# Kernel tuning notes

Measured on AMD Instinct MI355X. Metric: run time of the kernel, lower is better.

The kernel has to match this reference:

```python
import jax, jax.numpy as jnp
import numpy as np

NA, NPAPER, IN, HID, H, D, OUT, E = 16384, 16384, 128, 64, 4, 16, 349, 262144
NEG_SLOPE = 0.2  # DGL GATConv default leaky_relu slope


def _gat(hs, hd, src, dst, W, al, ar, b, n_dst):
    # DGL GATConv: shared fc, additive attention, edge softmax per dst, weighted sum.
    fs = (hs @ W).reshape(-1, H, D)            # [Ns,H,D]
    fd = (hd @ W).reshape(-1, H, D)            # [Nd,H,D]
    el = jnp.sum(fs * al, axis=-1)             # [Ns,H]
    er = jnp.sum(fd * ar, axis=-1)             # [Nd,H]
    e = jax.nn.leaky_relu(el[src] + er[dst], NEG_SLOPE)  # [E,H]
    m = jax.ops.segment_max(e, dst, num_segments=n_dst)
    m = jnp.where(jnp.isfinite(m), m, 0.0)
    ex = jnp.exp(e - m[dst])
    den = jax.ops.segment_sum(ex, dst, num_segments=n_dst)
    alpha = ex / jnp.maximum(den[dst], 1e-9)   # [E,H]
    out = jax.ops.segment_sum(fs[src] * alpha[..., None], dst, num_segments=n_dst)
    return out + b.reshape(1, H, D)


def _ln(x, g, b):
    m = jnp.mean(x, -1, keepdims=True)
    v = jnp.mean((x - m) ** 2, -1, keepdims=True)
    return (x - m) / jnp.sqrt(v + 1e-5) * g + b


def setup_inputs() -> dict:
    key = jax.random.key(0)
    ks = jax.random.split(key, 30)
    def n(k, shp, s=1.0):
        return jax.random.normal(ks[k], shp, jnp.float32) * s
    def ridx(k, hi):
        return jax.random.randint(ks[k], (E,), 0, hi)
    return dict(
        x_author=n(0, (NA, IN)), x_paper=n(1, (NPAPER, IN)),
        ntype_emb=n(2, (2, IN), 0.5),
        W0=n(3, (3, IN, HID), 0.1), al0=n(4, (3, H, D), 0.1), ar0=n(5, (3, H, D), 0.1), b0=jnp.zeros((3, HID), jnp.float32),
        W1=n(6, (3, HID, HID), 0.1), al1=n(7, (3, H, D), 0.1), ar1=n(8, (3, H, D), 0.1), b1=jnp.zeros((3, HID), jnp.float32),
        ln1_gb=jnp.array([1.0, 0.0], jnp.float32),
        attn_w=n(9, (4,), 0.5), attn_b=n(10, (4,), 0.1),
        ln2_gb=jnp.array([1.0, 0.0], jnp.float32),
        ffn_w1=n(11, (1, 16), 0.5), ffn_b1=jnp.zeros((16,), jnp.float32),
        ffn_w2=n(12, (16, 1), 0.5), ffn_b2=jnp.zeros((1,), jnp.float32),
        lin_W=n(13, (2 * HID, OUT), 0.1), lin_b=jnp.zeros((OUT,), jnp.float32),
        src_writes=ridx(14, NA), dst_writes=ridx(15, NPAPER),
        src_cites=ridx(16, NPAPER), dst_cites=ridx(17, NPAPER),
        src_revw=ridx(18, NPAPER), dst_revw=ridx(19, NA),
    )


def reference(x_author, x_paper, ntype_emb, W0, al0, ar0, b0, W1, al1, ar1, b1,
              ln1_gb, attn_w, attn_b, ln2_gb, ffn_w1, ffn_b1, ffn_w2, ffn_b2,
              lin_W, lin_b,
              src_writes, dst_writes, src_cites, dst_cites, src_revw, dst_revw):
    # node-type embedding scaling (x[nty] * ntype_emb[i])
    ha = x_author * ntype_emb[0]
    hp = x_paper * ntype_emb[1]

    def hetero(ha, hp, W, al, ar, b):
        # HeteroGraphConv with sum aggregation over etypes per dst ntype
        op = _gat(ha, hp, src_writes, dst_writes, W[0], al[0], ar[0], b[0], NPAPER) \
           + _gat(hp, hp, src_cites, dst_cites, W[1], al[1], ar[1], b[1], NPAPER)
        oa = _gat(hp, ha, src_revw, dst_revw, W[2], al[2], ar[2], b[2], NA)
        return oa.reshape(NA, HID), op.reshape(NPAPER, HID)

    ha, hp = hetero(ha, hp, W0, al0, ar0, b0)
    ha, hp = jax.nn.relu(ha), jax.nn.relu(hp)  # dropout = identity at eval
    ha, hp = hetero(ha, hp, W1, al1, ar1, b1)

    h1 = hp                                   # [NP, HID]
    x = h1[:, :, None]                        # [NP, HID, 1]: feature dims as tokens, d=1
    # DALayer (pre-LN transformer encoder layer, 1 head, d=1, scale=1)
    y = _ln(x, ln1_gb[0], ln1_gb[1])
    q = y * attn_w[0] + attn_b[0]
    k = y * attn_w[1] + attn_b[1]
    v = y * attn_w[2] + attn_b[2]
    att = jax.nn.softmax(jnp.einsum('nsd,ntd->nst', q, k), axis=-1)  # [NP,HID,HID]
    o = jnp.einsum('nst,ntd->nsd', att, v) * attn_w[3] + attn_b[3]
    x = x + o
    y = _ln(x, ln2_gb[0], ln2_gb[1])
    f = jax.nn.gelu(y @ ffn_w1 + ffn_b1, approximate=False) @ ffn_w2 + ffn_b2
    x = x + f
    h2 = x[:, :, 0]                           # squeeze

    def l2n(z):
        return z / jnp.maximum(jnp.linalg.norm(z, axis=1, keepdims=True), 1e-12)

    hf = jnp.concatenate([l2n(h1), l2n(h2)], axis=1)  # [NP, 2*HID]
    return hf @ lin_W + lin_b
```

## Files before the change

kernel.cpp:

```cpp
#include <hip/hip_runtime.h>
#include <math.h>

constexpr int N_A   = 16384;
constexpr int N_P   = 16384;
constexpr int IN_D  = 128;
constexpr int HID   = 64;
constexpr int NH    = 4;
constexpr int OUTD  = 349;
constexpr int NE    = 262144;
constexpr int NB    = 64;
constexpr float NEG = 0.2f;

__device__ __forceinline__ float lrelu(float x) { return x > 0.f ? x : NEG * x; }

__global__ __launch_bounds__(256) void k_chist(const int* __restrict__ dW, const int* __restrict__ dC,
                                               const int* __restrict__ dR, int* __restrict__ ccnt) {
    __shared__ int h[256];
    const int t = blockIdx.y;
    const int* __restrict__ d = t == 0 ? dW : t == 1 ? dC : dR;
    const int tid = threadIdx.x;
    h[tid] = 0;
    __syncthreads();
    const int base = blockIdx.x * 4096;
#pragma unroll
    for (int i = 0; i < 16; ++i) {
        int dst = d[base + i * 256 + tid];
        atomicAdd(&h[dst >> 6], 1);
    }
    __syncthreads();
    ccnt[(t * NB + blockIdx.x) * 256 + tid] = h[tid];
}

__global__ __launch_bounds__(768) void k_coffs(const int* __restrict__ ccnt, int* __restrict__ coffs,
                                               int* __restrict__ crow) {
    const int tid = threadIdx.x;
    const int t = tid >> 8, bin = tid & 255;
    int total = 0;
    for (int b = 0; b < NB; ++b) total += ccnt[(t * NB + b) * 256 + bin];
    __shared__ int sc[768];
    sc[tid] = total;
    __syncthreads();
    for (int w = 1; w < 256; w <<= 1) {
        int v = (bin >= w) ? sc[tid - w] : 0;
        __syncthreads();
        sc[tid] += v;
        __syncthreads();
    }
    const int incl = sc[tid];
    const int base = incl - total;
    crow[t * 257 + bin] = base;
    if (bin == 255) crow[t * 257 + 256] = incl;
    int run = base;
    for (int b = 0; b < NB; ++b) {
        int c = ccnt[(t * NB + b) * 256 + bin];
        coffs[(t * NB + b) * 256 + bin] = run;
        run += c;
    }
}

__global__ __launch_bounds__(256) void k_cscatter(const int* __restrict__ sW, const int* __restrict__ dW,
                                                  const int* __restrict__ sC, const int* __restrict__ dC,
                                                  const int* __restrict__ sR, const int* __restrict__ dR,
                                                  const int* __restrict__ coffs,
                                                  int* __restrict__ ebW, int* __restrict__ ebC,
                                                  int* __restrict__ ebR) {
    __shared__ int cur[256];
    const int t = blockIdx.y;
    const int* __restrict__ sp = t == 0 ? sW : t == 1 ? sC : sR;
    const int* __restrict__ dp = t == 0 ? dW : t == 1 ? dC : dR;
    int* __restrict__ eb = t == 0 ? ebW : t == 1 ? ebC : ebR;
    const int tid = threadIdx.x;
    cur[tid] = coffs[(t * NB + blockIdx.x) * 256 + tid];
    __syncthreads();
    const int base = blockIdx.x * 4096;
#pragma unroll
    for (int i = 0; i < 16; ++i) {
        int e = base + i * 256 + tid;
        int dst = dp[e], src = sp[e];
        int pos = atomicAdd(&cur[dst >> 6], 1);
        eb[pos] = src | ((dst & 63) << 14);
    }
}

__global__ __launch_bounds__(256) void k_fine(const int* __restrict__ crow,
                                              const int* __restrict__ ebW, const int* __restrict__ ebC,
                                              const int* __restrict__ ebR,
                                              int* __restrict__ row,
                                              int* __restrict__ esW, int* __restrict__ esC,
                                              int* __restrict__ esR) {
    __shared__ int bins[64], exc[64], cur[64];
    const int t = blockIdx.y, cb = blockIdx.x, tid = threadIdx.x;
    const int* __restrict__ eb = t == 0 ? ebW : t == 1 ? ebC : ebR;
    int* __restrict__ es = t == 0 ? esW : t == 1 ? esC : esR;
    const int lo = crow[t * 257 + cb], hi = crow[t * 257 + cb + 1];
    if (tid < 64) bins[tid] = 0;
    __syncthreads();
    for (int e = lo + tid; e < hi; e += 256) atomicAdd(&bins[eb[e] >> 14], 1);
    __syncthreads();
    if (tid == 0) {
        int r = 0;
#pragma unroll
        for (int j = 0; j < 64; ++j) { exc[j] = r; cur[j] = r; r += bins[j]; }
    }
    __syncthreads();
    if (tid < 64) row[t * 16385 + cb * 64 + tid] = lo + exc[tid];
    if (tid == 0 && cb == 255) row[t * 16385 + 16384] = crow[t * 257 + 256];
    for (int e = lo + tid; e < hi; e += 256) {
        int v = eb[e];
        int pos = atomicAdd(&cur[v >> 14], 1);
        es[lo + pos] = v & 16383;
    }
}

struct GemmJobs {
    const float* X[5];  const float* W[5];  const float* NT[5];
    float* F[5];        float* EL[5];       float* ER[5];
    const float* AL[5]; const float* AR[5];
};

template <int K, int RELU>
__global__ __launch_bounds__(256) void k_gemm(GemmJobs j) {
    __shared__ float Wc[32 * 64];
    __shared__ float XT[32][68];

    const float* __restrict__ X;  const float* __restrict__ Wp;  const float* __restrict__ NTp;
    float* __restrict__ F;  float* __restrict__ EL;  float* __restrict__ ER;
    const float* __restrict__ AL; const float* __restrict__ AR;
    switch (blockIdx.z) {
      case 0: X=j.X[0]; Wp=j.W[0]; NTp=j.NT[0]; F=j.F[0]; EL=j.EL[0]; ER=j.ER[0]; AL=j.AL[0]; AR=j.AR[0]; break;
      case 1: X=j.X[1]; Wp=j.W[1]; NTp=j.NT[1]; F=j.F[1]; EL=j.EL[1]; ER=j.ER[1]; AL=j.AL[1]; AR=j.AR[1]; break;
      case 2: X=j.X[2]; Wp=j.W[2]; NTp=j.NT[2]; F=j.F[2]; EL=j.EL[2]; ER=j.ER[2]; AL=j.AL[2]; AR=j.AR[2]; break;
      case 3: X=j.X[3]; Wp=j.W[3]; NTp=j.NT[3]; F=j.F[3]; EL=j.EL[3]; ER=j.ER[3]; AL=j.AL[3]; AR=j.AR[3]; break;
      default: X=j.X[4]; Wp=j.W[4]; NTp=j.NT[4]; F=j.F[4]; EL=j.EL[4]; ER=j.ER[4]; AL=j.AL[4]; AR=j.AR[4]; break;
    }

    const int tid = threadIdx.x;
    const int tx  = tid & 15;
    const int rg  = tid >> 4;
    const int r0  = blockIdx.x * 64;

    float acc[4][4] = {};

    for (int kc = 0; kc < K; kc += 32) {
        __syncthreads();
#pragma unroll
        for (int it = 0; it < 2; ++it) {
            int idx = tid * 4 + it * 1024;
            int k = idx >> 6, c = idx & 63;
            *(float4*)(Wc + idx) = *(const float4*)(Wp + (size_t)(kc + k) * 64 + c);
        }
#pragma unroll
        for (int it = 0; it < 2; ++it) {
            int idx = tid * 4 + it * 1024;
            int row = idx >> 5, col = idx & 31;
            float4 v = *(const float4*)(X + (size_t)(r0 + row) * K + kc + col);
            if (RELU) {
                v.x = fmaxf(v.x, 0.f); v.y = fmaxf(v.y, 0.f);
                v.z = fmaxf(v.z, 0.f); v.w = fmaxf(v.w, 0.f);
            }
            if (NTp) {
                float4 s = *(const float4*)(NTp + kc + col);
                v.x *= s.x; v.y *= s.y; v.z *= s.z; v.w *= s.w;
            }
            XT[col + 0][row] = v.x;
            XT[col + 1][row] = v.y;
            XT[col + 2][row] = v.z;
            XT[col + 3][row] = v.w;
        }
        __syncthreads();
#pragma unroll
        for (int kk = 0; kk < 32; ++kk) {
            float4 a4 = *(const float4*)(&XT[kk][rg * 4]);
            float4 w4 = *(const float4*)(Wc + kk * 64 + tx * 4);
            acc[0][0] = fmaf(a4.x, w4.x, acc[0][0]); acc[0][1] = fmaf(a4.x, w4.y, acc[0][1]);
            acc[0][2] = fmaf(a4.x, w4.z, acc[0][2]); acc[0][3] = fmaf(a4.x, w4.w, acc[0][3]);
            acc[1][0] = fmaf(a4.y, w4.x, acc[1][0]); acc[1][1] = fmaf(a4.y, w4.y, acc[1][1]);
            acc[1][2] = fmaf(a4.y, w4.z, acc[1][2]); acc[1][3] = fmaf(a4.y, w4.w, acc[1][3]);
            acc[2][0] = fmaf(a4.z, w4.x, acc[2][0]); acc[2][1] = fmaf(a4.z, w4.y, acc[2][1]);
            acc[2][2] = fmaf(a4.z, w4.z, acc[2][2]); acc[2][3] = fmaf(a4.z, w4.w, acc[2][3]);
            acc[3][0] = fmaf(a4.w, w4.x, acc[3][0]); acc[3][1] = fmaf(a4.w, w4.y, acc[3][1]);
            acc[3][2] = fmaf(a4.w, w4.z, acc[3][2]); acc[3][3] = fmaf(a4.w, w4.w, acc[3][3]);
        }
    }

    if (F) {
#pragma unroll
        for (int i = 0; i < 4; ++i) {
            size_t n = (size_t)r0 + rg * 4 + i;
            *(float4*)(F + n * 64 + tx * 4) =
                make_float4(acc[i][0], acc[i][1], acc[i][2], acc[i][3]);
        }
    }
    if (EL) {
        float4 alv = ((const float4*)AL)[tx];
#pragma unroll
        for (int i = 0; i < 4; ++i) {
            float p = acc[i][0] * alv.x + acc[i][1] * alv.y +
                      acc[i][2] * alv.z + acc[i][3] * alv.w;
            p += __shfl_xor(p, 1, 64);
            p += __shfl_xor(p, 2, 64);
            if ((tx & 3) == 0) EL[((size_t)r0 + rg * 4 + i) * 4 + (tx >> 2)] = p;
        }
    }
    if (ER) {
        float4 arv = ((const float4*)AR)[tx];
#pragma unroll
        for (int i = 0; i < 4; ++i) {
            float p = acc[i][0] * arv.x + acc[i][1] * arv.y +
                      acc[i][2] * arv.z + acc[i][3] * arv.w;
            p += __shfl_xor(p, 1, 64);
            p += __shfl_xor(p, 2, 64);
            if ((tx & 3) == 0) ER[((size_t)r0 + rg * 4 + i) * 4 + (tx >> 2)] = p;
        }
    }
}

struct AggType { const int* row; const int* es; const float* el; const float* er; const float* fs; };
struct AggArgs {
    AggType t[3]; const float* b; float* op; float* oa;
    float* hf;
    const float* ln1gb; const float* aw; const float* ab; const float* ln2gb;
    const float* fw1; const float* fb1; const float* fw2; const float* fb2;
};

__device__ __forceinline__ float4 agg16v(const int* __restrict__ rowv, const int* __restrict__ es,
                                         const float* __restrict__ el, const float* __restrict__ er,
                                         const float* __restrict__ fs, int d, int lane,
                                         float* denOut) {
    float4 acc = make_float4(0.f, 0.f, 0.f, 0.f);
    float den = 0.f;
    int start = rowv[d], deg = rowv[d + 1] - start;
    if (deg > 0) {
        const int j16 = lane & 15;
        const int g   = lane >> 4;
        const int h   = j16 >> 2;
        const float rh = er[(size_t)d * 4 + g];
        for (int e0 = 0; e0 < deg; e0 += 16) {
            int o = e0 + j16;
            int sn = es[start + (o < deg ? o : 0)];
            float wv = 0.f;
            if (o < deg) wv = __expf(lrelu(el[(size_t)sn * 4 + g] + rh));
            den += wv;
#pragma unroll
            for (int sub = 0; sub < 4; ++sub) {
                int eidx = sub * 4 + g;
                int snj  = __shfl(sn, eidx, 64);
                float wj = __shfl(wv, (h << 4) + eidx, 64);
                float4 f4 = *(const float4*)(fs + (size_t)snj * 64 + j16 * 4);
                acc.x = fmaf(wj, f4.x, acc.x);
                acc.y = fmaf(wj, f4.y, acc.y);
                acc.z = fmaf(wj, f4.z, acc.z);
                acc.w = fmaf(wj, f4.w, acc.w);
            }
        }
    }
    *denOut = den;
    return acc;
}

__device__ __forceinline__ float4 agg_finish(float4 acc, float den, int lane) {
#pragma unroll
    for (int w = 1; w < 16; w <<= 1) den += __shfl_xor(den, w, 64);
#pragma unroll
    for (int w = 16; w < 64; w <<= 1) {
        acc.x += __shfl_xor(acc.x, w, 64);
        acc.y += __shfl_xor(acc.y, w, 64);
        acc.z += __shfl_xor(acc.z, w, 64);
        acc.w += __shfl_xor(acc.w, w, 64);
    }
    float denh = __shfl(den, (((lane & 15) >> 2) << 4), 64);
    float inv = 1.f / fmaxf(denh, 1e-9f);
    acc.x *= inv; acc.y *= inv; acc.z *= inv; acc.w *= inv;
    return acc;
}

template <int L1>
__global__ __launch_bounds__(256) void k_agg(AggArgs A) {
    int wid = (blockIdx.x * 256 + threadIdx.x) >> 6;
    int lane = threadIdx.x & 63;
    int c16 = lane & 15;
    if (L1 == 0) {
        if (wid < N_P) {
            float d0, d1;
            float4 a0 = agg16v(A.t[0].row, A.t[0].es, A.t[0].el, A.t[0].er, A.t[0].fs, wid, lane, &d0);
            float4 a1 = agg16v(A.t[1].row, A.t[1].es, A.t[1].el, A.t[1].er, A.t[1].fs, wid, lane, &d1);
            a0 = agg_finish(a0, d0, lane);
            a1 = agg_finish(a1, d1, lane);
            if (lane < 16) {
                float4 b0 = *(const float4*)(A.b + c16 * 4);
                float4 b1 = *(const float4*)(A.b + 64 + c16 * 4);
                float4 o = make_float4(a0.x + a1.x + b0.x + b1.x,
                                       a0.y + a1.y + b0.y + b1.y,
                                       a0.z + a1.z + b0.z + b1.z,
                                       a0.w + a1.w + b0.w + b1.w);
                *(float4*)(A.op + (size_t)wid * 64 + c16 * 4) = o;
            }
        } else {
            int d = wid - N_P;
            float d2;
            float4 a2 = agg16v(A.t[2].row, A.t[2].es, A.t[2].el, A.t[2].er, A.t[2].fs, d, lane, &d2);
            a2 = agg_finish(a2, d2, lane);
            if (lane < 16) {
                float4 b2 = *(const float4*)(A.b + 128 + c16 * 4);
                float4 o = make_float4(a2.x + b2.x, a2.y + b2.y, a2.z + b2.z, a2.w + b2.w);
                *(float4*)(A.oa + (size_t)d * 64 + c16 * 4) = o;
            }
        }
    } else {
        float d0, d1;
        float4 a0 = agg16v(A.t[0].row, A.t[0].es, A.t[0].el, A.t[0].er, A.t[0].fs, wid, lane, &d0);
        float4 a1 = agg16v(A.t[1].row, A.t[1].es, A.t[1].el, A.t[1].er, A.t[1].fs, wid, lane, &d1);
        a0 = agg_finish(a0, d0, lane);
        a1 = agg_finish(a1, d1, lane);
        float4 b0 = *(const float4*)(A.b + c16 * 4);
        float4 b1 = *(const float4*)(A.b + 64 + c16 * 4);
        float4 o = make_float4(a0.x + a1.x + b0.x + b1.x,
                               a0.y + a1.y + b0.y + b1.y,
                               a0.z + a1.z + b0.z + b1.z,
                               a0.w + a1.w + b0.w + b1.w);
        float y1 = A.ln1gb[1];
        float vv = y1 * A.aw[2] + A.ab[2];
        float oo = vv * A.aw[3] + A.ab[3];
        float y2 = A.ln2gb[1];
        float f  = A.fb2[0];
#pragma unroll
        for (int q = 0; q < 16; ++q) {
            float zz = y2 * A.fw1[q] + A.fb1[q];
            f += 0.5f * zz * (1.f + erff(zz * 0.70710678118654752f)) * A.fw2[q];
        }
        float C = oo + f;
        float4 oc = make_float4(o.x + C, o.y + C, o.z + C, o.w + C);
        float s1 = o.x * o.x + o.y * o.y + o.z * o.z + o.w * o.w;
        float s2 = oc.x * oc.x + oc.y * oc.y + oc.z * oc.z + oc.w * oc.w;
#pragma unroll
        for (int w = 1; w < 16; w <<= 1) {
            s1 += __shfl_xor(s1, w, 64);
            s2 += __shfl_xor(s2, w, 64);
        }
        float i1 = 1.f / fmaxf(sqrtf(s1), 1e-12f);
        float i2 = 1.f / fmaxf(sqrtf(s2), 1e-12f);
        if (lane < 16) {
            *(float4*)(A.hf + (size_t)wid * 128 + c16 * 4) =
                make_float4(o.x * i1, o.y * i1, o.z * i1, o.w * i1);
            *(float4*)(A.hf + (size_t)wid * 128 + 64 + c16 * 4) =
                make_float4(oc.x * i2, oc.y * i2, oc.z * i2, oc.w * i2);
        }
    }
}

__global__ __launch_bounds__(256) void k_gemm_out(const float* __restrict__ X,
                                                  const float* __restrict__ W,
                                                  const float* __restrict__ bias,
                                                  float* __restrict__ out) {
    __shared__ float Wc[32 * 64];
    __shared__ float XT[32][68];
    const int tid = threadIdx.x;
    const int tx  = tid & 15;
    const int rg  = tid >> 4;
    const int r0  = blockIdx.x * 64;
    const int c0  = blockIdx.y * 64;

    float acc[4][4] = {};

    for (int kc = 0; kc < 128; kc += 32) {
        __syncthreads();
#pragma unroll
        for (int it = 0; it < 2; ++it) {
            int idx = tid * 4 + it * 1024;
            int k = idx >> 6, c = idx & 63;
            int gk = kc + k;
            float4 v;
            int gc = c0 + c;
            v.x = (gc + 0 < OUTD) ? W[(size_t)gk * OUTD + gc + 0] : 0.f;
            v.y = (gc + 1 < OUTD) ? W[(size_t)gk * OUTD + gc + 1] : 0.f;
            v.z = (gc + 2 < OUTD) ? W[(size_t)gk * OUTD + gc + 2] : 0.f;
            v.w = (gc + 3 < OUTD) ? W[(size_t)gk * OUTD + gc + 3] : 0.f;
            *(float4*)(Wc + idx) = v;
        }
#pragma unroll
        for (int it = 0; it < 2; ++it) {
            int idx = tid * 4 + it * 1024;
            int row = idx >> 5, col = idx & 31;
            float4 v = *(const float4*)(X + (size_t)(r0 + row) * 128 + kc + col);
            XT[col + 0][row] = v.x;
            XT[col + 1][row] = v.y;
            XT[col + 2][row] = v.z;
            XT[col + 3][row] = v.w;
        }
        __syncthreads();
#pragma unroll
        for (int kk = 0; kk < 32; ++kk) {
            float4 a4 = *(const float4*)(&XT[kk][rg * 4]);
            float4 w4 = *(const float4*)(Wc + kk * 64 + tx * 4);
            acc[0][0] = fmaf(a4.x, w4.x, acc[0][0]); acc[0][1] = fmaf(a4.x, w4.y, acc[0][1]);
            acc[0][2] = fmaf(a4.x, w4.z, acc[0][2]); acc[0][3] = fmaf(a4.x, w4.w, acc[0][3]);
            acc[1][0] = fmaf(a4.y, w4.x, acc[1][0]); acc[1][1] = fmaf(a4.y, w4.y, acc[1][1]);
            acc[1][2] = fmaf(a4.y, w4.z, acc[1][2]); acc[1][3] = fmaf(a4.y, w4.w, acc[1][3]);
            acc[2][0] = fmaf(a4.z, w4.x, acc[2][0]); acc[2][1] = fmaf(a4.z, w4.y, acc[2][1]);
            acc[2][2] = fmaf(a4.z, w4.z, acc[2][2]); acc[2][3] = fmaf(a4.z, w4.w, acc[2][3]);
            acc[3][0] = fmaf(a4.w, w4.x, acc[3][0]); acc[3][1] = fmaf(a4.w, w4.y, acc[3][1]);
            acc[3][2] = fmaf(a4.w, w4.z, acc[3][2]); acc[3][3] = fmaf(a4.w, w4.w, acc[3][3]);
        }
    }

    float b4[4];
#pragma unroll
    for (int q = 0; q < 4; ++q) {
        int c = c0 + tx * 4 + q;
        b4[q] = (c < OUTD) ? bias[c] : 0.f;
    }
#pragma unroll
    for (int i = 0; i < 4; ++i) {
        size_t n = (size_t)r0 + rg * 4 + i;
#pragma unroll
        for (int q = 0; q < 4; ++q) {
            int c = c0 + tx * 4 + q;
            if (c < OUTD) out[n * OUTD + c] = acc[i][q] + b4[q];
        }
    }
}

extern "C" void kernel_launch(void* const* d_in, const int* in_sizes, int n_in,
                              void* d_out, int out_size, void* d_ws, size_t ws_size,
                              hipStream_t stream) {
    const float* x_author = (const float*)d_in[0];
    const float* x_paper  = (const float*)d_in[1];
    const float* ntype    = (const float*)d_in[2];
    const float* W0  = (const float*)d_in[3];
    const float* al0 = (const float*)d_in[4];
    const float* ar0 = (const float*)d_in[5];
    const float* b0  = (const float*)d_in[6];
    const float* W1  = (const float*)d_in[7];
    const float* al1 = (const float*)d_in[8];
    const float* ar1 = (const float*)d_in[9];
    const float* b1  = (const float*)d_in[10];
    const float* ln1gb = (const float*)d_in[11];
    const float* attw  = (const float*)d_in[12];
    const float* attb  = (const float*)d_in[13];
    const float* ln2gb = (const float*)d_in[14];
    const float* fw1 = (const float*)d_in[15];
    const float* fb1 = (const float*)d_in[16];
    const float* fw2 = (const float*)d_in[17];
    const float* fb2 = (const float*)d_in[18];
    const float* linW = (const float*)d_in[19];
    const float* linb = (const float*)d_in[20];
    const int* srcW = (const int*)d_in[21];
    const int* dstW = (const int*)d_in[22];
    const int* srcC = (const int*)d_in[23];
    const int* dstC = (const int*)d_in[24];
    const int* srcR = (const int*)d_in[25];
    const int* dstR = (const int*)d_in[26];
    float* out = (float*)d_out;

    float* ws = (float*)d_ws;
    size_t off = 0;
    float* fsW = ws + off; off += (size_t)N_A * HID;
    float* fsC = ws + off; off += (size_t)N_P * HID;
    float* fsR = ws + off; off += (size_t)N_P * HID;
    float* elw = ws + off; off += (size_t)N_A * NH;
    float* erw = ws + off; off += (size_t)N_P * NH;
    float* elc = ws + off; off += (size_t)N_P * NH;
    float* erc = ws + off; off += (size_t)N_P * NH;
    float* elr = ws + off; off += (size_t)N_P * NH;
    float* err = ws + off; off += (size_t)N_A * NH;
    float* oa0 = ws + off; off += (size_t)N_A * HID;
    float* op0 = ws + off; off += (size_t)N_P * HID;
    float* hf  = ws + off; off += (size_t)N_P * 2 * HID;
    int* ccnt  = (int*)(ws + off); off += 3 * NB * 256;
    int* coffs = (int*)(ws + off); off += 3 * NB * 256;
    int* crow  = (int*)(ws + off); off += 3 * 257 + 1;
    int* row   = (int*)(ws + off); off += 3 * 16385 + 1;
    int* ebW  = (int*)(ws + off); off += NE;
    int* ebC  = (int*)(ws + off); off += NE;
    int* ebR  = (int*)(ws + off); off += NE;
    int* esW  = (int*)(ws + off); off += NE;
    int* esC  = (int*)(ws + off); off += NE;
    int* esR  = (int*)(ws + off); off += NE;

    const int* rowW = row;
    const int* rowC = row + 16385;
    const int* rowR = row + 2 * 16385;

    const float* ntA = ntype;
    const float* ntP = ntype + IN_D;

    GemmJobs j0{};
    j0.X[0] = x_author; j0.W[0] = W0;                  j0.NT[0] = ntA;
    j0.F[0] = fsW; j0.EL[0] = elw; j0.ER[0] = nullptr; j0.AL[0] = al0;       j0.AR[0] = nullptr;
    j0.X[1] = x_paper;  j0.W[1] = W0;                  j0.NT[1] = ntP;
    j0.F[1] = nullptr; j0.EL[1] = nullptr; j0.ER[1] = erw; j0.AL[1] = nullptr; j0.AR[1] = ar0;
    j0.X[2] = x_paper;  j0.W[2] = W0 + IN_D * HID;     j0.NT[2] = ntP;
    j0.F[2] = fsC; j0.EL[2] = elc; j0.ER[2] = erc;     j0.AL[2] = al0 + 64;  j0.AR[2] = ar0 + 64;
    j0.X[3] = x_paper;  j0.W[3] = W0 + 2 * IN_D * HID; j0.NT[3] = ntP;
    j0.F[3] = fsR; j0.EL[3] = elr; j0.ER[3] = nullptr; j0.AL[3] = al0 + 128; j0.AR[3] = nullptr;
    j0.X[4] = x_author; j0.W[4] = W0 + 2 * IN_D * HID; j0.NT[4] = ntA;
    j0.F[4] = nullptr; j0.EL[4] = nullptr; j0.ER[4] = err; j0.AL[4] = nullptr; j0.AR[4] = ar0 + 128;

    GemmJobs j1{};
    j1.X[0] = oa0; j1.W[0] = W1;                   j1.NT[0] = nullptr;
    j1.F[0] = fsW; j1.EL[0] = elw; j1.ER[0] = nullptr; j1.AL[0] = al1;       j1.AR[0] = nullptr;
    j1.X[1] = op0; j1.W[1] = W1;                   j1.NT[1] = nullptr;
    j1.F[1] = nullptr; j1.EL[1] = nullptr; j1.ER[1] = erw; j1.AL[1] = nullptr; j1.AR[1] = ar1;
    j1.X[2] = op0; j1.W[2] = W1 + HID * HID;       j1.NT[2] = nullptr;
    j1.F[2] = fsC; j1.EL[2] = elc; j1.ER[2] = erc;     j1.AL[2] = al1 + 64;  j1.AR[2] = ar1 + 64;

    AggArgs a0{};
    a0.t[0] = {rowW, esW, elw, erw, fsW};
    a0.t[1] = {rowC, esC, elc, erc, fsC};
    a0.t[2] = {rowR, esR, elr, err, fsR};
    a0.b = b0; a0.op = op0; a0.oa = oa0;
    AggArgs a1 = a0;
    a1.b = b1; a1.op = nullptr; a1.oa = nullptr;
    a1.hf = hf;
    a1.ln1gb = ln1gb; a1.aw = attw; a1.ab = attb; a1.ln2gb = ln2gb;
    a1.fw1 = fw1; a1.fb1 = fb1; a1.fw2 = fw2; a1.fb2 = fb2;

    k_chist<<<dim3(NB, 3), 256, 0, stream>>>(dstW, dstC, dstR, ccnt);
    k_coffs<<<1, 768, 0, stream>>>(ccnt, coffs, crow);
    k_cscatter<<<dim3(NB, 3), 256, 0, stream>>>(srcW, dstW, srcC, dstC, srcR, dstR,
                                                coffs, ebW, ebC, ebR);
    k_fine<<<dim3(256, 3), 256, 0, stream>>>(crow, ebW, ebC, ebR, row, esW, esC, esR);

    k_gemm<IN_D, 0><<<dim3(N_A / 64, 1, 5), 256, 0, stream>>>(j0);
    k_agg<0><<<(N_P + N_A) / 4, 256, 0, stream>>>(a0);

    k_gemm<HID, 1><<<dim3(N_A / 64, 1, 3), 256, 0, stream>>>(j1);
    k_agg<1><<<N_P / 4, 256, 0, stream>>>(a1);

    k_gemm_out<<<dim3(N_P / 64, (OUTD + 63) / 64), 256, 0, stream>>>(hf, linW, linb, out);
}
```

Before: 148.9 us.

## Share input tile across projection jobs per node type; enlarge output GEMM row tile

```diff
diff --git a/kernel.cpp b/kernel.cpp
--- a/kernel.cpp
+++ b/kernel.cpp
@@ -112,42 +112,34 @@
     }
 }
 
-struct GemmJobs {
-    const float* X[5];  const float* W[5];  const float* NT[5];
-    float* F[5];        float* EL[5];       float* ER[5];
-    const float* AL[5]; const float* AR[5];
+struct GJob { const float* W; float* F; float* EL; float* ER; const float* AL; const float* AR; };
+struct G2Args {
+    const float* XA; const float* NTA; GJob ja[3];
+    const float* XP; const float* NTP; GJob jp[3];
 };
 
-template <int K, int RELU>
-__global__ __launch_bounds__(256) void k_gemm(GemmJobs j) {
-    __shared__ float Wc[32 * 64];
-    __shared__ float XT[32][68];
-
-    const float* __restrict__ X;  const float* __restrict__ Wp;  const float* __restrict__ NTp;
-    float* __restrict__ F;  float* __restrict__ EL;  float* __restrict__ ER;
-    const float* __restrict__ AL; const float* __restrict__ AR;
-    switch (blockIdx.z) {
-      case 0: X=j.X[0]; Wp=j.W[0]; NTp=j.NT[0]; F=j.F[0]; EL=j.EL[0]; ER=j.ER[0]; AL=j.AL[0]; AR=j.AR[0]; break;
-      case 1: X=j.X[1]; Wp=j.W[1]; NTp=j.NT[1]; F=j.F[1]; EL=j.EL[1]; ER=j.ER[1]; AL=j.AL[1]; AR=j.AR[1]; break;
-      case 2: X=j.X[2]; Wp=j.W[2]; NTp=j.NT[2]; F=j.F[2]; EL=j.EL[2]; ER=j.ER[2]; AL=j.AL[2]; AR=j.AR[2]; break;
-      case 3: X=j.X[3]; Wp=j.W[3]; NTp=j.NT[3]; F=j.F[3]; EL=j.EL[3]; ER=j.ER[3]; AL=j.AL[3]; AR=j.AR[3]; break;
-      default: X=j.X[4]; Wp=j.W[4]; NTp=j.NT[4]; F=j.F[4]; EL=j.EL[4]; ER=j.ER[4]; AL=j.AL[4]; AR=j.AR[4]; break;
-    }
-
+template <int K, int RELU, int NJ, bool AUT>
+__device__ __forceinline__ void gemm_core(const G2Args& g, float* WcBase, float (*XT)[68]) {
+    const float* __restrict__ X  = AUT ? g.XA : g.XP;
+    const float* __restrict__ NTp = AUT ? g.NTA : g.NTP;
     const int tid = threadIdx.x;
     const int tx  = tid & 15;
     const int rg  = tid >> 4;
     const int r0  = blockIdx.x * 64;
 
-    float acc[4][4] = {};
+    float acc[NJ][4][4] = {};
 
     for (int kc = 0; kc < K; kc += 32) {
         __syncthreads();
 #pragma unroll
-        for (int it = 0; it < 2; ++it) {
-            int idx = tid * 4 + it * 1024;
-            int k = idx >> 6, c = idx & 63;
-            *(float4*)(Wc + idx) = *(const float4*)(Wp + (size_t)(kc + k) * 64 + c);
+        for (int j = 0; j < NJ; ++j) {
+            const float* Wp = AUT ? g.ja[j].W : g.jp[j].W;
+#pragma unroll
+            for (int it = 0; it < 2; ++it) {
+                int idx = tid * 4 + it * 1024;
+                int k = idx >> 6, c = idx & 63;
+                *(float4*)(WcBase + j * 2048 + idx) = *(const float4*)(Wp + (size_t)(kc + k) * 64 + c);
+            }
         }
 #pragma unroll
         for (int it = 0; it < 2; ++it) {
@@ -171,48 +163,68 @@
 #pragma unroll
         for (int kk = 0; kk < 32; ++kk) {
             float4 a4 = *(const float4*)(&XT[kk][rg * 4]);
-            float4 w4 = *(const float4*)(Wc + kk * 64 + tx * 4);
-            acc[0][0] = fmaf(a4.x, w4.x, acc[0][0]); acc[0][1] = fmaf(a4.x, w4.y, acc[0][1]);
-            acc[0][2] = fmaf(a4.x, w4.z, acc[0][2]); acc[0][3] = fmaf(a4.x, w4.w, acc[0][3]);
-            acc[1][0] = fmaf(a4.y, w4.x, acc[1][0]); acc[1][1] = fmaf(a4.y, w4.y, acc[1][1]);
-            acc[1][2] = fmaf(a4.y, w4.z, acc[1][2]); acc[1][3] = fmaf(a4.y, w4.w, acc[1][3]);
-            acc[2][0] = fmaf(a4.z, w4.x, acc[2][0]); acc[2][1] = fmaf(a4.z, w4.y, acc[2][1]);
-            acc[2][2] = fmaf(a4.z, w4.z, acc[2][2]); acc[2][3] = fmaf(a4.z, w4.w, acc[2][3]);
-            acc[3][0] = fmaf(a4.w, w4.x, acc[3][0]); acc[3][1] = fmaf(a4.w, w4.y, acc[3][1]);
-            acc[3][2] = fmaf(a4.w, w4.z, acc[3][2]); acc[3][3] = fmaf(a4.w, w4.w, acc[3][3]);
-        }
-    }
-
-    if (F) {
-#pragma unroll
-        for (int i = 0; i < 4; ++i) {
-            size_t n = (size_t)r0 + rg * 4 + i;
-            *(float4*)(F + n * 64 + tx * 4) =
-                make_float4(acc[i][0], acc[i][1], acc[i][2], acc[i][3]);
-        }
-    }
-    if (EL) {
-        float4 alv = ((const float4*)AL)[tx];
-#pragma unroll
-        for (int i = 0; i < 4; ++i) {
-            float p = acc[i][0] * alv.x + acc[i][1] * alv.y +
-                      acc[i][2] * alv.z + acc[i][3] * alv.w;
-            p += __shfl_xor(p, 1, 64);
-            p += __shfl_xor(p, 2, 64);
-            if ((tx & 3) == 0) EL[((size_t)r0 + rg * 4 + i) * 4 + (tx >> 2)] = p;
-        }
-    }
-    if (ER) {
-        float4 arv = ((const float4*)AR)[tx];
-#pragma unroll
-        for (int i = 0; i < 4; ++i) {
-            float p = acc[i][0] * arv.x + acc[i][1] * arv.y +
-                      acc[i][2] * arv.z + acc[i][3] * arv.w;
-            p += __shfl_xor(p, 1, 64);
-            p += __shfl_xor(p, 2, 64);
-            if ((tx & 3) == 0) ER[((size_t)r0 + rg * 4 + i) * 4 + (tx >> 2)] = p;
-        }
-    }
+#pragma unroll
+            for (int j = 0; j < NJ; ++j) {
+                float4 w4 = *(const float4*)(WcBase + j * 2048 + kk * 64 + tx * 4);
+                acc[j][0][0] = fmaf(a4.x, w4.x, acc[j][0][0]); acc[j][0][1] = fmaf(a4.x, w4.y, acc[j][0][1]);
+                acc[j][0][2] = fmaf(a4.x, w4.z, acc[j][0][2]); acc[j][0][3] = fmaf(a4.x, w4.w, acc[j][0][3]);
+                acc[j][1][0] = fmaf(a4.y, w4.x, acc[j][1][0]); acc[j][1][1] = fmaf(a4.y, w4.y, acc[j][1][1]);
+                acc[j][1][2] = fmaf(a4.y, w4.z, acc[j][1][2]); acc[j][1][3] = fmaf(a4.y, w4.w, acc[j][1][3]);
+                acc[j][2][0] = fmaf(a4.z, w4.x, acc[j][2][0]); acc[j][2][1] = fmaf(a4.z, w4.y, acc[j][2][1]);
+                acc[j][2][2] = fmaf(a4.z, w4.z, acc[j][2][2]); acc[j][2][3] = fmaf(a4.z, w4.w, acc[j][2][3]);
+                acc[j][3][0] = fmaf(a4.w, w4.x, acc[j][3][0]); acc[j][3][1] = fmaf(a4.w, w4.y, acc[j][3][1]);
+                acc[j][3][2] = fmaf(a4.w, w4.z, acc[j][3][2]); acc[j][3][3] = fmaf(a4.w, w4.w, acc[j][3][3]);
+            }
+        }
+    }
+
+#pragma unroll
+    for (int j = 0; j < NJ; ++j) {
+        float* F  = AUT ? g.ja[j].F  : g.jp[j].F;
+        float* EL = AUT ? g.ja[j].EL : g.jp[j].EL;
+        float* ER = AUT ? g.ja[j].ER : g.jp[j].ER;
+        const float* AL = AUT ? g.ja[j].AL : g.jp[j].AL;
+        const float* AR = AUT ? g.ja[j].AR : g.jp[j].AR;
+        if (F) {
+#pragma unroll
+            for (int i = 0; i < 4; ++i) {
+                size_t n = (size_t)r0 + rg * 4 + i;
+                *(float4*)(F + n * 64 + tx * 4) =
+                    make_float4(acc[j][i][0], acc[j][i][1], acc[j][i][2], acc[j][i][3]);
+            }
+        }
+        if (EL) {
+            float4 alv = ((const float4*)AL)[tx];
+#pragma unroll
+            for (int i = 0; i < 4; ++i) {
+                float p = acc[j][i][0] * alv.x + acc[j][i][1] * alv.y +
+                          acc[j][i][2] * alv.z + acc[j][i][3] * alv.w;
+                p += __shfl_xor(p, 1, 64);
+                p += __shfl_xor(p, 2, 64);
+                if ((tx & 3) == 0) EL[((size_t)r0 + rg * 4 + i) * 4 + (tx >> 2)] = p;
+            }
+        }
+        if (ER) {
+            float4 arv = ((const float4*)AR)[tx];
+#pragma unroll
+            for (int i = 0; i < 4; ++i) {
+                float p = acc[j][i][0] * arv.x + acc[j][i][1] * arv.y +
+                          acc[j][i][2] * arv.z + acc[j][i][3] * arv.w;
+                p += __shfl_xor(p, 1, 64);
+                p += __shfl_xor(p, 2, 64);
+                if ((tx & 3) == 0) ER[((size_t)r0 + rg * 4 + i) * 4 + (tx >> 2)] = p;
+            }
+        }
+    }
+}
+
+template <int K, int RELU, int NJA, int NJP>
+__global__ __launch_bounds__(256) void k_gemm2(G2Args g) {
+    constexpr int MJ = (NJA > NJP) ? NJA : NJP;
+    __shared__ float Wc[MJ * 2048];
+    __shared__ float XT[32][68];
+    if (blockIdx.z == 0) gemm_core<K, RELU, NJA, true>(g, Wc, XT);
+    else                 gemm_core<K, RELU, NJP, false>(g, Wc, XT);
 }
 
 struct AggType { const int* row; const int* es; const float* el; const float* er; const float* fs; };
@@ -353,14 +365,14 @@
                                                   const float* __restrict__ bias,
                                                   float* __restrict__ out) {
     __shared__ float Wc[32 * 64];
-    __shared__ float XT[32][68];
+    __shared__ float XT[32][132];
     const int tid = threadIdx.x;
     const int tx  = tid & 15;
     const int rg  = tid >> 4;
-    const int r0  = blockIdx.x * 64;
+    const int r0  = blockIdx.x * 128;
     const int c0  = blockIdx.y * 64;
 
-    float acc[4][4] = {};
+    float acc[8][4] = {};
 
     for (int kc = 0; kc < 128; kc += 32) {
         __syncthreads();
@@ -378,7 +390,7 @@
             *(float4*)(Wc + idx) = v;
         }
 #pragma unroll
-        for (int it = 0; it < 2; ++it) {
+        for (int it = 0; it < 4; ++it) {
             int idx = tid * 4 + it * 1024;
             int row = idx >> 5, col = idx & 31;
             float4 v = *(const float4*)(X + (size_t)(r0 + row) * 128 + kc + col);
@@ -390,16 +402,25 @@
         __syncthreads();
 #pragma unroll
         for (int kk = 0; kk < 32; ++kk) {
-            float4 a4 = *(const float4*)(&XT[kk][rg * 4]);
+            float4 a0 = *(const float4*)(&XT[kk][rg * 8]);
+            float4 a1 = *(const float4*)(&XT[kk][rg * 8 + 4]);
             float4 w4 = *(const float4*)(Wc + kk * 64 + tx * 4);
-            acc[0][0] = fmaf(a4.x, w4.x, acc[0][0]); acc[0][1] = fmaf(a4.x, w4.y, acc[0][1]);
-            acc[0][2] = fmaf(a4.x, w4.z, acc[0][2]); acc[0][3] = fmaf(a4.x, w4.w, acc[0][3]);
-            acc[1][0] = fmaf(a4.y, w4.x, acc[1][0]); acc[1][1] = fmaf(a4.y, w4.y, acc[1][1]);
-            acc[1][2] = fmaf(a4.y, w4.z, acc[1][2]); acc[1][3] = fmaf(a4.y, w4.w, acc[1][3]);
-            acc[2][0] = fmaf(a4.z, w4.x, acc[2][0]); acc[2][1] = fmaf(a4.z, w4.y, acc[2][1]);
-            acc[2][2] = fmaf(a4.z, w4.z, acc[2][2]); acc[2][3] = fmaf(a4.z, w4.w, acc[2][3]);
-            acc[3][0] = fmaf(a4.w, w4.x, acc[3][0]); acc[3][1] = fmaf(a4.w, w4.y, acc[3][1]);
-            acc[3][2] = fmaf(a4.w, w4.z, acc[3][2]); acc[3][3] = fmaf(a4.w, w4.w, acc[3][3]);
+            acc[0][0] = fmaf(a0.x, w4.x, acc[0][0]); acc[0][1] = fmaf(a0.x, w4.y, acc[0][1]);
+            acc[0][2] = fmaf(a0.x, w4.z, acc[0][2]); acc[0][3] = fmaf(a0.x, w4.w, acc[0][3]);
+            acc[1][0] = fmaf(a0.y, w4.x, acc[1][0]); acc[1][1] = fmaf(a0.y, w4.y, acc[1][1]);
+            acc[1][2] = fmaf(a0.y, w4.z, acc[1][2]); acc[1][3] = fmaf(a0.y, w4.w, acc[1][3]);
+            acc[2][0] = fmaf(a0.z, w4.x, acc[2][0]); acc[2][1] = fmaf(a0.z, w4.y, acc[2][1]);
+            acc[2][2] = fmaf(a0.z, w4.z, acc[2][2]); acc[2][3] = fmaf(a0.z, w4.w, acc[2][3]);
+            acc[3][0] = fmaf(a0.w, w4.x, acc[3][0]); acc[3][1] = fmaf(a0.w, w4.y, acc[3][1]);
+            acc[3][2] = fmaf(a0.w, w4.z, acc[3][2]); acc[3][3] = fmaf(a0.w, w4.w, acc[3][3]);
+            acc[4][0] = fmaf(a1.x, w4.x, acc[4][0]); acc[4][1] = fmaf(a1.x, w4.y, acc[4][1]);
+            acc[4][2] = fmaf(a1.x, w4.z, acc[4][2]); acc[4][3] = fmaf(a1.x, w4.w, acc[4][3]);
+            acc[5][0] = fmaf(a1.y, w4.x, acc[5][0]); acc[5][1] = fmaf(a1.y, w4.y, acc[5][1]);
+            acc[5][2] = fmaf(a1.y, w4.z, acc[5][2]); acc[5][3] = fmaf(a1.y, w4.w, acc[5][3]);
+            acc[6][0] = fmaf(a1.z, w4.x, acc[6][0]); acc[6][1] = fmaf(a1.z, w4.y, acc[6][1]);
+            acc[6][2] = fmaf(a1.z, w4.z, acc[6][2]); acc[6][3] = fmaf(a1.z, w4.w, acc[6][3]);
+            acc[7][0] = fmaf(a1.w, w4.x, acc[7][0]); acc[7][1] = fmaf(a1.w, w4.y, acc[7][1]);
+            acc[7][2] = fmaf(a1.w, w4.z, acc[7][2]); acc[7][3] = fmaf(a1.w, w4.w, acc[7][3]);
         }
     }
 
@@ -410,8 +431,8 @@
         b4[q] = (c < OUTD) ? bias[c] : 0.f;
     }
 #pragma unroll
-    for (int i = 0; i < 4; ++i) {
-        size_t n = (size_t)r0 + rg * 4 + i;
+    for (int i = 0; i < 8; ++i) {
+        size_t n = (size_t)r0 + rg * 8 + i;
 #pragma unroll
         for (int q = 0; q < 4; ++q) {
             int c = c0 + tx * 4 + q;
@@ -484,25 +505,21 @@
     const float* ntA = ntype;
     const float* ntP = ntype + IN_D;
 
-    GemmJobs j0{};
-    j0.X[0] = x_author; j0.W[0] = W0;                  j0.NT[0] = ntA;
-    j0.F[0] = fsW; j0.EL[0] = elw; j0.ER[0] = nullptr; j0.AL[0] = al0;       j0.AR[0] = nullptr;
-    j0.X[1] = x_paper;  j0.W[1] = W0;                  j0.NT[1] = ntP;
-    j0.F[1] = nullptr; j0.EL[1] = nullptr; j0.ER[1] = erw; j0.AL[1] = nullptr; j0.AR[1] = ar0;
-    j0.X[2] = x_paper;  j0.W[2] = W0 + IN_D * HID;     j0.NT[2] = ntP;
-    j0.F[2] = fsC; j0.EL[2] = elc; j0.ER[2] = erc;     j0.AL[2] = al0 + 64;  j0.AR[2] = ar0 + 64;
-    j0.X[3] = x_paper;  j0.W[3] = W0 + 2 * IN_D * HID; j0.NT[3] = ntP;
-    j0.F[3] = fsR; j0.EL[3] = elr; j0.ER[3] = nullptr; j0.AL[3] = al0 + 128; j0.AR[3] = nullptr;
-    j0.X[4] = x_author; j0.W[4] = W0 + 2 * IN_D * HID; j0.NT[4] = ntA;
-    j0.F[4] = nullptr; j0.EL[4] = nullptr; j0.ER[4] = err; j0.AL[4] = nullptr; j0.AR[4] = ar0 + 128;
-
-    GemmJobs j1{};
-    j1.X[0] = oa0; j1.W[0] = W1;                   j1.NT[0] = nullptr;
-    j1.F[0] = fsW; j1.EL[0] = elw; j1.ER[0] = nullptr; j1.AL[0] = al1;       j1.AR[0] = nullptr;
-    j1.X[1] = op0; j1.W[1] = W1;                   j1.NT[1] = nullptr;
-    j1.F[1] = nullptr; j1.EL[1] = nullptr; j1.ER[1] = erw; j1.AL[1] = nullptr; j1.AR[1] = ar1;
-    j1.X[2] = op0; j1.W[2] = W1 + HID * HID;       j1.NT[2] = nullptr;
-    j1.F[2] = fsC; j1.EL[2] = elc; j1.ER[2] = erc;     j1.AL[2] = al1 + 64;  j1.AR[2] = ar1 + 64;
+    G2Args g0{};
+    g0.XA = x_author; g0.NTA = ntA;
+    g0.ja[0] = {W0,                    fsW,     elw,     nullptr, al0,       nullptr};
+    g0.ja[1] = {W0 + 2 * IN_D * HID,   nullptr, nullptr, err,     nullptr,   ar0 + 128};
+    g0.XP = x_paper; g0.NTP = ntP;
+    g0.jp[0] = {W0,                    nullptr, nullptr, erw,     nullptr,   ar0};
+    g0.jp[1] = {W0 + IN_D * HID,       fsC,     elc,     erc,     al0 + 64,  ar0 + 64};
+    g0.jp[2] = {W0 + 2 * IN_D * HID,   fsR,     elr,     nullptr, al0 + 128, nullptr};
+
+    G2Args g1{};
+    g1.XA = oa0; g1.NTA = nullptr;
+    g1.ja[0] = {W1,                    fsW,     elw,     nullptr, al1,       nullptr};
+    g1.XP = op0; g1.NTP = nullptr;
+    g1.jp[0] = {W1,                    nullptr, nullptr, erw,     nullptr,   ar1};
+    g1.jp[1] = {W1 + HID * HID,        fsC,     elc,     erc,     al1 + 64,  ar1 + 64};
 
     AggArgs a0{};
     a0.t[0] = {rowW, esW, elw, erw, fsW};
@@ -521,11 +538,11 @@
                                                 coffs, ebW, ebC, ebR);
     k_fine<<<dim3(256, 3), 256, 0, stream>>>(crow, ebW, ebC, ebR, row, esW, esC, esR);
 
-    k_gemm<IN_D, 0><<<dim3(N_A / 64, 1, 5), 256, 0, stream>>>(j0);
+    k_gemm2<IN_D, 0, 2, 3><<<dim3(N_A / 64, 1, 2), 256, 0, stream>>>(g0);
     k_agg<0><<<(N_P + N_A) / 4, 256, 0, stream>>>(a0);
 
-    k_gemm<HID, 1><<<dim3(N_A / 64, 1, 3), 256, 0, stream>>>(j1);
+    k_gemm2<HID, 1, 1, 2><<<dim3(N_A / 64, 1, 2), 256, 0, stream>>>(g1);
     k_agg<1><<<N_P / 4, 256, 0, stream>>>(a1);
 
-    k_gemm_out<<<dim3(N_P / 64, (OUTD + 63) / 64), 256, 0, stream>>>(hf, linW, linb, out);
-}
+    k_gemm_out<<<dim3(N_P / 128, (OUTD + 63) / 64), 256, 0, stream>>>(hf, linW, linb, out);
+}
```

Result: slower. 156.9 us (+5.4%).
